# Optimization experiments

Measured on AMD Instinct MI355X. Metric: run time of the kernel, lower is better.

Reference implementation:

```python
import jax, jax.numpy as jnp
import numpy as np

N_WRD = 2000
WCODE = 3
EMB = 32
VSIZE = 7
VIEW = (16, 16)
B = 64
CSIZE = 128


def _vcode():
    # torch.meshgrid with default 'ij' indexing, cat -> (2, H*W) -> (H*W, 2)
    x = jnp.linspace(-1.0, 1.0, VIEW[0])
    y = jnp.linspace(-1.0, 1.0, VIEW[1])
    xg, yg = jnp.meshgrid(x, y, indexing='ij')
    return jnp.stack([xg.reshape(-1), yg.reshape(-1)], axis=-1)  # (V, 2)


def setup_inputs() -> dict:
    key = jax.random.key(0)
    ks = jax.random.split(key, 20)
    s = 0.02
    d = {
        'view_cell': jax.random.normal(ks[0], (B, CSIZE, VIEW[0] * VIEW[1]), jnp.float32),
        'v': jax.random.normal(ks[1], (B, VSIZE), jnp.float32),
        'w2c_w1': jax.random.normal(ks[2], (VSIZE, 512), jnp.float32) * s,
        'w2c_b1': jnp.zeros((512,), jnp.float32),
        'w2c_w2': jax.random.normal(ks[3], (512, WCODE * N_WRD), jnp.float32) * s,
        'w2c_b2': jnp.zeros((WCODE * N_WRD,), jnp.float32),
        'fc1_w': jax.random.normal(ks[4], (WCODE, 256), jnp.float32) * s,
        'fc1_b': jnp.zeros((256,), jnp.float32),
        'fc2_w': jax.random.normal(ks[5], (256, 256), jnp.float32) * s,
        'fc2_b': jnp.zeros((256,), jnp.float32),
        'fca_w': jax.random.normal(ks[6], (256, 1), jnp.float32) * s,
        'fca_b': jnp.zeros((1,), jnp.float32),
        'fce_w': jax.random.normal(ks[7], (256, EMB), jnp.float32) * s,
        'fce_b': jnp.zeros((EMB,), jnp.float32),
        'vse_w1': jax.random.normal(ks[8], (2, 128), jnp.float32) * s,
        'vse_b1': jnp.zeros((128,), jnp.float32),
        'vse_w2': jax.random.normal(ks[9], (128, EMB), jnp.float32) * s,
        'vse_b2': jnp.zeros((EMB,), jnp.float32),
    }
    return d


def reference(view_cell, v, w2c_w1, w2c_b1, w2c_w2, w2c_b2,
              fc1_w, fc1_b, fc2_w, fc2_b, fca_w, fca_b, fce_w, fce_b,
              vse_w1, vse_b1, vse_w2, vse_b2):
    b = v.shape[0]
    # w2c: v -> per-cell world codes
    h0 = jax.nn.relu(v @ w2c_w1 + w2c_b1)                     # (B, 512)
    wcode = (h0 @ w2c_w2 + w2c_b2).reshape(-1, WCODE)          # (B*N, 3)
    h = jax.nn.relu(wcode @ fc1_w + fc1_b)                     # (B*N, 256)
    h = jax.nn.relu(h @ fc2_w + fc2_b)
    activation = jax.nn.sigmoid(h @ fca_w + fca_b).reshape(b, N_WRD, 1)
    cs_emb = (h @ fce_w + fce_b).reshape(b, N_WRD, EMB)        # (B, N, E)
    # view-space embedding of the pixel grid
    vcode = _vcode()                                           # (V, 2)
    vs = jax.nn.relu(vcode @ vse_w1 + vse_b1) @ vse_w2 + vse_b2  # (V, E)
    # relation / gated softmax routing
    relation = jnp.einsum('bne,ve->bnv', cs_emb, vs)           # (B, N, V)
    route = jax.nn.softmax(relation, axis=2) * activation      # (B, N, V)
    # write: view_cell (B, C, V) @ route^T (B, V, N) -> (B, C, N)
    wrd_cell = jnp.einsum('bcv,bnv->bcn', view_cell, route)
    return wrd_cell
```

## Files before the change

### kernel.cpp

```cpp
#include <hip/hip_runtime.h>
#include <hip/hip_bf16.h>
#include <math.h>

#define NWRD 2000
#define BB 64
#define CS 128
#define VV 256

typedef __attribute__((ext_vector_type(8)))  short short8;
typedef __attribute__((ext_vector_type(16))) float f32x16;

#define WS_FC2WT 0
#define WS_WCODE (WS_FC2WT + 32768)
#define WS_VSB   (WS_WCODE + 384000)
#define WS_W2T   (WS_VSB + 4096)
#define WS_VCB   (WS_W2T + 1536000)
#define WS_FCEWT (WS_VCB + 1048576)
#define WS_H0B   (WS_FCEWT + 4096)
#define WS_FCAWB (WS_H0B + 16384)

__device__ __forceinline__ unsigned short f2bf(float x) {
    unsigned int u = __float_as_uint(x);
    u += 0x7fffu + ((u >> 16) & 1u);
    return (unsigned short)(u >> 16);
}

#define PREP_A 1024
#define PREP_B (PREP_A + 752)
#define PREP_C (PREP_B + 128)
#define PREP_D (PREP_C + 32)
#define PREP_E (PREP_D + 16)
#define PREP_N (PREP_E + 1)
__global__ __launch_bounds__(256) void kprep(
        const float* __restrict__ vc, unsigned short* __restrict__ vcb,
        const float* __restrict__ w2, unsigned short* __restrict__ w2T,
        const float* __restrict__ v, const float* __restrict__ w2c_w1,
        const float* __restrict__ w2c_b1, unsigned short* __restrict__ h0b,
        const float* __restrict__ vse_w1, const float* __restrict__ vse_b1,
        const float* __restrict__ vse_w2, const float* __restrict__ vse_b2,
        unsigned short* __restrict__ vsb,
        const float* __restrict__ fc2_w, unsigned short* __restrict__ fc2wT,
        const float* __restrict__ fce_w, unsigned short* __restrict__ fcewT,
        const float* __restrict__ fca_w, unsigned short* __restrict__ fcawB) {
    __shared__ unsigned short smem[9216];
    int bid = blockIdx.x, t = threadIdx.x;
    if (bid < PREP_A) {
        int i = (bid * 256 + t) * 8;
        float4 f0 = *(const float4*)(vc + i);
        float4 f1 = *(const float4*)(vc + i + 4);
        union { short8 v8; unsigned short u[8]; } o;
        o.u[0] = f2bf(f0.x); o.u[1] = f2bf(f0.y); o.u[2] = f2bf(f0.z); o.u[3] = f2bf(f0.w);
        o.u[4] = f2bf(f1.x); o.u[5] = f2bf(f1.y); o.u[6] = f2bf(f1.z); o.u[7] = f2bf(f1.w);
        *(short8*)(vcb + i) = o.v8;
    } else if (bid < PREP_B) {
        unsigned short (*tile)[66] = (unsigned short(*)[66])smem;
        int b2 = bid - PREP_A;
        int n0 = (b2 % 94) * 64, k0 = (b2 / 94) * 64;
        int nl = t & 63, kb = (t >> 6) * 16;
        int nc = (n0 + nl) < 6000 ? (n0 + nl) : 5999;
#pragma unroll
        for (int i = 0; i < 16; i++)
            tile[nl][kb + i] = f2bf(w2[(size_t)(k0 + kb + i)*6000 + nc]);
        __syncthreads();
        int kl = t & 63, nb = (t >> 6) * 16;
#pragma unroll
        for (int i = 0; i < 16; i++) {
            int nn = n0 + nb + i;
            if (nn < 6000) w2T[(size_t)nn*512 + k0 + kl] = tile[nb + i][kl];
        }
    } else if (bid < PREP_C) {
        int c = bid - PREP_B;
        int b = c >> 1, j = (c & 1)*256 + t;
        float s = w2c_b1[j];
#pragma unroll
        for (int k = 0; k < 7; k++) s = fmaf(v[b*7 + k], w2c_w1[k*512 + j], s);
        h0b[b*512 + j] = f2bf(fmaxf(s, 0.f));
    } else if (bid < PREP_D) {
        float* hs = (float*)smem;
        int blk = bid - PREP_C;
        int m = t & 127, half = t >> 7;
#pragma unroll
        for (int q = 0; q < 4; q++) {
            int vloc = half*4 + q;
            int vv = blk*8 + vloc;
            float x = (2.f/15.f)*(float)(vv >> 4) - 1.f;
            float y = (2.f/15.f)*(float)(vv & 15) - 1.f;
            float h = vse_b1[m] + x*vse_w1[m] + y*vse_w1[128 + m];
            hs[vloc*128 + m] = fmaxf(h, 0.f);
        }
        __syncthreads();
        int vloc = t >> 5, e = t & 31;
        float s = vse_b2[e];
        for (int mm = 0; mm < 128; mm++) s = fmaf(hs[vloc*128 + mm], vse_w2[mm*32 + e], s);
        vsb[(blk*8 + vloc)*32 + e] = f2bf(s);
    } else if (bid < PREP_E) {
        unsigned short (*tile)[72] = (unsigned short(*)[72])smem;
        int b2 = bid - PREP_D;
        int k0t = (b2 >> 2) * 64, n0t = (b2 & 3) * 64;
        int nl = t & 63, kb = (t >> 6) * 16;
#pragma unroll
        for (int i = 0; i < 16; i++)
            tile[kb + i][nl] = f2bf(fc2_w[(size_t)(k0t + kb + i)*256 + n0t + nl]);
        __syncthreads();
        int kl = t & 63, nb = (t >> 6) * 16;
#pragma unroll
        for (int i = 0; i < 16; i++)
            fc2wT[(size_t)(n0t + nb + i)*256 + k0t + kl] = tile[kl][nb + i];
    } else {
        int e = t & 31, kb = (t >> 5) * 32;
        unsigned short tmp[32];
#pragma unroll
        for (int i = 0; i < 32; i++) tmp[i] = f2bf(fce_w[(size_t)(kb + i)*32 + e]);
#pragma unroll
        for (int i = 0; i < 4; i++)
            *(short8*)(fcewT + (size_t)e*256 + kb + i*8) = *(short8*)(tmp + i*8);
#pragma unroll
        for (int i = 0; i < 32; i++)
            fcawB[(size_t)e*256 + kb + i] = (e == 0) ? f2bf(fca_w[kb + i]) : (unsigned short)0;
    }
}

__global__ __launch_bounds__(512) void k2_gemm(const unsigned short* __restrict__ h0b,
        const unsigned short* __restrict__ w2T, const float* __restrict__ b2,
        float* __restrict__ wcode) {
    int t = threadIdx.x;
    int w = t >> 6, lane = t & 63, l31 = lane & 31, h = lane >> 5;
    int mt = w & 1, nt = w >> 1;
    int n = blockIdx.x*128 + nt*32 + l31;
    int nc = n < 6000 ? n : 5999;
    f32x16 a0v, a1v;
#pragma unroll
    for (int i = 0; i < 16; i++) { a0v[i] = 0.f; a1v[i] = 0.f; }
#pragma unroll 8
    for (int ks = 0; ks < 16; ks++) {
        int k0 = ks*16 + h*8;
        short8 af0 = *(const short8*)(h0b + (mt*32 + l31)*512 + k0);
        short8 bf0 = *(const short8*)(w2T + (size_t)nc*512 + k0);
        a0v = __builtin_amdgcn_mfma_f32_32x32x16_bf16(af0, bf0, a0v, 0, 0, 0);
        short8 af1 = *(const short8*)(h0b + (mt*32 + l31)*512 + k0 + 256);
        short8 bf1 = *(const short8*)(w2T + (size_t)nc*512 + k0 + 256);
        a1v = __builtin_amdgcn_mfma_f32_32x32x16_bf16(af1, bf1, a1v, 0, 0, 0);
    }
    if (n < 6000) {
        float bias = b2[n];
#pragma unroll
        for (int i = 0; i < 16; i++) {
            int row = (i & 3) + 8*(i >> 2) + 4*h;
            wcode[(size_t)(mt*32 + row)*6000 + n] = a0v[i] + a1v[i] + bias;
        }
    }
}

#define K45_LDS 77056
__global__ __launch_bounds__(512, 4) void k45(
        const unsigned short* __restrict__ vcb,
        const float* __restrict__ wcode,
        const float* __restrict__ fc1_w, const float* __restrict__ fc1_b,
        const unsigned short* __restrict__ fc2wT, const float* __restrict__ fc2_b,
        const float* __restrict__ fca_b_p,
        const unsigned short* __restrict__ fcawB,
        const unsigned short* __restrict__ fcewT, const float* __restrict__ fce_b,
        const unsigned short* __restrict__ vsb,
        float* __restrict__ out) {
    extern __shared__ char lds[];
    unsigned short* h1b    = (unsigned short*)lds;
    unsigned short* h2b    = (unsigned short*)(lds + 33792);
    unsigned short* routeB = h2b;
    unsigned short* embL   = (unsigned short*)(lds + 67584);
    float* actL   = (float*)(lds + 72704);
    float* wcsAll = (float*)(lds + 72960);
    float* redS   = (float*)(lds + 76032);
    int t = threadIdx.x;
    int w = t >> 6, lane = t & 63, l31 = lane & 31, h = lane >> 5;
    int b = blockIdx.y;
    int n0 = blockIdx.x * 256;

    {
        const float* wb = wcode + (size_t)b*6000;
        int i0 = n0*3 + t;
        wcsAll[t] = wb[i0 < 6000 ? i0 : 5999];
        if (t < 256) {
            int i1 = n0*3 + 512 + t;
            wcsAll[512 + t] = wb[i1 < 6000 ? i1 : 5999];
        }
    }
    int jq = (t & 63) * 4;
    float4 wa  = *(const float4*)(fc1_w + jq);
    float4 wb4 = *(const float4*)(fc1_w + 256 + jq);
    float4 wc  = *(const float4*)(fc1_w + 512 + jq);
    float4 bb4 = *(const float4*)(fc1_b + jq);
    int mtA = w & 1, na = (w >> 1) * 32, nb2 = na + 128;
    float ba = fc2_b[na + l31], bbv = fc2_b[nb2 + l31];
    float be = fce_b[l31];
    float fcab = fca_b_p[0];
    int ntR = w & 1, vq = w >> 1;
    int ctE = w >> 1, ntE = w & 1;
    size_t arowE = ((size_t)(b*128 + ctE*32 + l31))*256;
    __syncthreads();

    for (int c = 0; c < 4; c++) {
        int w0 = n0 + c*64;
#pragma unroll
        for (int rr = 0; rr < 8; rr++) {
            int r = w*8 + rr;
            const float* wr = wcsAll + (c*64 + r)*3;
            float c0 = wr[0], c1 = wr[1], c2 = wr[2];
            float v0 = fmaxf(fmaf(c2, wc.x, fmaf(c1, wb4.x, fmaf(c0, wa.x, bb4.x))), 0.f);
            float v1 = fmaxf(fmaf(c2, wc.y, fmaf(c1, wb4.y, fmaf(c0, wa.y, bb4.y))), 0.f);
            float v2 = fmaxf(fmaf(c2, wc.z, fmaf(c1, wb4.z, fmaf(c0, wa.z, bb4.z))), 0.f);
            float v3 = fmaxf(fmaf(c2, wc.w, fmaf(c1, wb4.w, fmaf(c0, wa.w, bb4.w))), 0.f);
            uint2 p;
            p.x = (unsigned int)f2bf(v0) | ((unsigned int)f2bf(v1) << 16);
            p.y = (unsigned int)f2bf(v2) | ((unsigned int)f2bf(v3) << 16);
            *(uint2*)(h1b + r*264 + jq) = p;
        }
        __syncthreads();
        {
            f32x16 c0, c1;
#pragma unroll
            for (int i = 0; i < 16; i++) { c0[i] = 0.f; c1[i] = 0.f; }
#pragma unroll 4
            for (int ks = 0; ks < 16; ks++) {
                int k0 = ks*16 + h*8;
                short8 af  = *(const short8*)(h1b + (mtA*32 + l31)*264 + k0);
                short8 bfa = *(const short8*)(fc2wT + (size_t)(na  + l31)*256 + k0);
                short8 bfb = *(const short8*)(fc2wT + (size_t)(nb2 + l31)*256 + k0);
                c0 = __builtin_amdgcn_mfma_f32_32x32x16_bf16(af, bfa, c0, 0, 0, 0);
                c1 = __builtin_amdgcn_mfma_f32_32x32x16_bf16(af, bfb, c1, 0, 0, 0);
            }
#pragma unroll
            for (int i = 0; i < 16; i++) {
                int row = (i & 3) + 8*(i >> 2) + 4*h;
                h2b[(mtA*32 + row)*264 + na  + l31] = f2bf(fmaxf(c0[i] + ba, 0.f));
                h2b[(mtA*32 + row)*264 + nb2 + l31] = f2bf(fmaxf(c1[i] + bbv, 0.f));
            }
        }
        __syncthreads();
        if (w < 2) {
            f32x16 ce;
#pragma unroll
            for (int i = 0; i < 16; i++) ce[i] = 0.f;
#pragma unroll 4
            for (int ks = 0; ks < 16; ks++) {
                int k0 = ks*16 + h*8;
                short8 af = *(const short8*)(h2b + (w*32 + l31)*264 + k0);
                short8 bf = *(const short8*)(fcewT + (size_t)l31*256 + k0);
                ce = __builtin_amdgcn_mfma_f32_32x32x16_bf16(af, bf, ce, 0, 0, 0);
            }
#pragma unroll
            for (int i = 0; i < 16; i++) {
                int row = (i & 3) + 8*(i >> 2) + 4*h;
                embL[(w*32 + row)*40 + l31] = f2bf(ce[i] + be);
            }
        } else if (w < 4) {
            int m = w - 2;
            f32x16 ca;
#pragma unroll
            for (int i = 0; i < 16; i++) ca[i] = 0.f;
#pragma unroll 4
            for (int ks = 0; ks < 16; ks++) {
                int k0 = ks*16 + h*8;
                short8 af = *(const short8*)(h2b + (m*32 + l31)*264 + k0);
                short8 bf = *(const short8*)(fcawB + (size_t)l31*256 + k0);
                ca = __builtin_amdgcn_mfma_f32_32x32x16_bf16(af, bf, ca, 0, 0, 0);
            }
            if (l31 == 0) {
#pragma unroll
                for (int i = 0; i < 16; i++) {
                    int row = (i & 3) + 8*(i >> 2) + 4*h;
                    actL[m*32 + row] = 1.f / (1.f + __expf(-(ca[i] + fcab)));
                }
            }
        }
        __syncthreads();
        int nloc = ntR*32 + l31;
        f32x16 ra[2];
#pragma unroll
        for (int mt = 0; mt < 2; mt++)
#pragma unroll
            for (int i = 0; i < 16; i++) ra[mt][i] = 0.f;
#pragma unroll
        for (int s = 0; s < 2; s++) {
            short8 bfrag = *(const short8*)(embL + nloc*40 + s*16 + h*8);
#pragma unroll
            for (int mt = 0; mt < 2; mt++) {
                int vrow = (vq*2 + mt)*32 + l31;
                short8 afrag = *(const short8*)(vsb + vrow*32 + s*16 + h*8);
                ra[mt] = __builtin_amdgcn_mfma_f32_32x32x16_bf16(afrag, bfrag, ra[mt], 0, 0, 0);
            }
        }
        float sm = 0.f;
#pragma unroll
        for (int mt = 0; mt < 2; mt++)
#pragma unroll
            for (int i = 0; i < 16; i++) {
                float e = __expf(ra[mt][i]);
                ra[mt][i] = e;
                sm += e;
            }
        sm += __shfl_xor(sm, 32);
        if (lane < 32) redS[w*32 + l31] = sm;
        __syncthreads();
        sm = 0.f;
#pragma unroll
        for (int q = 0; q < 4; q++) sm += redS[(q*2 + ntR)*32 + l31];
        float scale = actL[nloc] / sm;
#pragma unroll
        for (int mt = 0; mt < 2; mt++) {
#pragma unroll
            for (int rp = 0; rp < 4; rp++) {
                int vb = (vq*2 + mt)*32 + rp*8 + h*4;
                unsigned int p0 = (unsigned int)f2bf(ra[mt][rp*4+0]*scale)
                                | ((unsigned int)f2bf(ra[mt][rp*4+1]*scale) << 16);
                unsigned int p1 = (unsigned int)f2bf(ra[mt][rp*4+2]*scale)
                                | ((unsigned int)f2bf(ra[mt][rp*4+3]*scale) << 16);
                *(uint2*)(routeB + nloc*264 + vb) = make_uint2(p0, p1);
            }
        }
        __syncthreads();
        {
            f32x16 cc;
#pragma unroll
            for (int i = 0; i < 16; i++) cc[i] = 0.f;
            const unsigned short* rrow = routeB + (ntE*32 + l31)*264;
#pragma unroll 4
            for (int ks = 0; ks < 16; ks++) {
                int k0 = ks*16 + h*8;
                short8 bf = *(const short8*)(rrow + k0);
                short8 a0 = *(const short8*)(vcb + arowE + k0);
                cc = __builtin_amdgcn_mfma_f32_32x32x16_bf16(a0, bf, cc, 0, 0, 0);
            }
            int ng = w0 + ntE*32 + l31;
            if (ng < NWRD) {
                float* ob = out + (size_t)b*128*NWRD + ng;
#pragma unroll
                for (int i = 0; i < 16; i++) {
                    int crow = (i & 3) + 8*(i >> 2) + 4*h;
                    ob[(size_t)(ctE*32 + crow)*NWRD] = cc[i];
                }
            }
        }
    }
}

extern "C" void kernel_launch(void* const* d_in, const int* in_sizes, int n_in,
                              void* d_out, int out_size, void* d_ws, size_t ws_size,
                              hipStream_t stream) {
    const float* view_cell = (const float*)d_in[0];
    const float* v       = (const float*)d_in[1];
    const float* w2c_w1  = (const float*)d_in[2];
    const float* w2c_b1  = (const float*)d_in[3];
    const float* w2c_w2  = (const float*)d_in[4];
    const float* w2c_b2  = (const float*)d_in[5];
    const float* fc1_w   = (const float*)d_in[6];
    const float* fc1_b   = (const float*)d_in[7];
    const float* fc2_w   = (const float*)d_in[8];
    const float* fc2_b   = (const float*)d_in[9];
    const float* fca_w   = (const float*)d_in[10];
    const float* fca_b   = (const float*)d_in[11];
    const float* fce_w   = (const float*)d_in[12];
    const float* fce_b   = (const float*)d_in[13];
    const float* vse_w1  = (const float*)d_in[14];
    const float* vse_b1  = (const float*)d_in[15];
    const float* vse_w2  = (const float*)d_in[16];
    const float* vse_b2  = (const float*)d_in[17];
    float* ws    = (float*)d_ws;
    unsigned short* fc2wT = (unsigned short*)(ws + WS_FC2WT);
    float* wcode = ws + WS_WCODE;
    unsigned short* vsb   = (unsigned short*)(ws + WS_VSB);
    unsigned short* w2T   = (unsigned short*)(ws + WS_W2T);
    unsigned short* vcb   = (unsigned short*)(ws + WS_VCB);
    unsigned short* fcewT = (unsigned short*)(ws + WS_FCEWT);
    unsigned short* h0b   = (unsigned short*)(ws + WS_H0B);
    unsigned short* fcawB = (unsigned short*)(ws + WS_FCAWB);
    float* out   = (float*)d_out;

    kprep<<<PREP_N, 256, 0, stream>>>(view_cell, vcb, w2c_w2, w2T,
                                      v, w2c_w1, w2c_b1, h0b,
                                      vse_w1, vse_b1, vse_w2, vse_b2, vsb,
                                      fc2_w, fc2wT, fce_w, fcewT, fca_w, fcawB);
    k2_gemm<<<47, 512, 0, stream>>>(h0b, w2T, w2c_b2, wcode);
    (void)hipFuncSetAttribute((const void*)k45,
                              hipFuncAttributeMaxDynamicSharedMemorySize, K45_LDS);
    dim3 g45(8, 64);
    k45<<<g45, 512, K45_LDS, stream>>>(vcb, wcode, fc1_w, fc1_b, fc2wT, fc2_b,
                                       fca_b, fcawB, fcewT, fce_b, vsb, out);
}
```

Before: 243.9 us.

## Fuse w2 transpose and h0 compute into LDS-staged GEMM; defer softmax normalization

Removes the separate w2 transpose and h0 passes through global workspace. A new kernel converts w2 columns to bf16 directly in LDS, computes h0 per block in LDS, and runs the full K=512 MFMA GEMM from LDS. Separately, the softmax normalization and activation scale are moved from the per-element route packing to the output epilogue, which removes one __syncthreads in k45. The trade-off is that h0 is recomputed in each of 94 blocks and the w2 reads are strided per column.

```diff
diff --git a/kernel.cpp b/kernel.cpp
--- a/kernel.cpp
+++ b/kernel.cpp
@@ -13,11 +13,9 @@
 #define WS_FC2WT 0
 #define WS_WCODE (WS_FC2WT + 32768)
 #define WS_VSB   (WS_WCODE + 384000)
-#define WS_W2T   (WS_VSB + 4096)
-#define WS_VCB   (WS_W2T + 1536000)
+#define WS_VCB   (WS_VSB + 4096)
 #define WS_FCEWT (WS_VCB + 1048576)
-#define WS_H0B   (WS_FCEWT + 4096)
-#define WS_FCAWB (WS_H0B + 16384)
+#define WS_FCAWB (WS_FCEWT + 4096)
 
 __device__ __forceinline__ unsigned short f2bf(float x) {
     unsigned int u = __float_as_uint(x);
@@ -25,17 +23,12 @@
     return (unsigned short)(u >> 16);
 }
 
-#define PREP_A 1024
-#define PREP_B (PREP_A + 752)
-#define PREP_C (PREP_B + 128)
-#define PREP_D (PREP_C + 32)
-#define PREP_E (PREP_D + 16)
-#define PREP_N (PREP_E + 1)
-__global__ __launch_bounds__(256) void kprep(
+#define PL_A 1024
+#define PL_B (PL_A + 32)
+#define PL_C (PL_B + 16)
+#define PL_N (PL_C + 1)
+__global__ __launch_bounds__(256) void kprep_light(
         const float* __restrict__ vc, unsigned short* __restrict__ vcb,
-        const float* __restrict__ w2, unsigned short* __restrict__ w2T,
-        const float* __restrict__ v, const float* __restrict__ w2c_w1,
-        const float* __restrict__ w2c_b1, unsigned short* __restrict__ h0b,
         const float* __restrict__ vse_w1, const float* __restrict__ vse_b1,
         const float* __restrict__ vse_w2, const float* __restrict__ vse_b2,
         unsigned short* __restrict__ vsb,
@@ -44,7 +37,7 @@
         const float* __restrict__ fca_w, unsigned short* __restrict__ fcawB) {
     __shared__ unsigned short smem[9216];
     int bid = blockIdx.x, t = threadIdx.x;
-    if (bid < PREP_A) {
+    if (bid < PL_A) {
         int i = (bid * 256 + t) * 8;
         float4 f0 = *(const float4*)(vc + i);
         float4 f1 = *(const float4*)(vc + i + 4);
@@ -52,32 +45,9 @@
         o.u[0] = f2bf(f0.x); o.u[1] = f2bf(f0.y); o.u[2] = f2bf(f0.z); o.u[3] = f2bf(f0.w);
         o.u[4] = f2bf(f1.x); o.u[5] = f2bf(f1.y); o.u[6] = f2bf(f1.z); o.u[7] = f2bf(f1.w);
         *(short8*)(vcb + i) = o.v8;
-    } else if (bid < PREP_B) {
-        unsigned short (*tile)[66] = (unsigned short(*)[66])smem;
-        int b2 = bid - PREP_A;
-        int n0 = (b2 % 94) * 64, k0 = (b2 / 94) * 64;
-        int nl = t & 63, kb = (t >> 6) * 16;
-        int nc = (n0 + nl) < 6000 ? (n0 + nl) : 5999;
-#pragma unroll
-        for (int i = 0; i < 16; i++)
-            tile[nl][kb + i] = f2bf(w2[(size_t)(k0 + kb + i)*6000 + nc]);
-        __syncthreads();
-        int kl = t & 63, nb = (t >> 6) * 16;
-#pragma unroll
-        for (int i = 0; i < 16; i++) {
-            int nn = n0 + nb + i;
-            if (nn < 6000) w2T[(size_t)nn*512 + k0 + kl] = tile[nb + i][kl];
-        }
-    } else if (bid < PREP_C) {
-        int c = bid - PREP_B;
-        int b = c >> 1, j = (c & 1)*256 + t;
-        float s = w2c_b1[j];
-#pragma unroll
-        for (int k = 0; k < 7; k++) s = fmaf(v[b*7 + k], w2c_w1[k*512 + j], s);
-        h0b[b*512 + j] = f2bf(fmaxf(s, 0.f));
-    } else if (bid < PREP_D) {
+    } else if (bid < PL_B) {
         float* hs = (float*)smem;
-        int blk = bid - PREP_C;
+        int blk = bid - PL_A;
         int m = t & 127, half = t >> 7;
 #pragma unroll
         for (int q = 0; q < 4; q++) {
@@ -93,9 +63,9 @@
         float s = vse_b2[e];
         for (int mm = 0; mm < 128; mm++) s = fmaf(hs[vloc*128 + mm], vse_w2[mm*32 + e], s);
         vsb[(blk*8 + vloc)*32 + e] = f2bf(s);
-    } else if (bid < PREP_E) {
+    } else if (bid < PL_C) {
         unsigned short (*tile)[72] = (unsigned short(*)[72])smem;
-        int b2 = bid - PREP_D;
+        int b2 = bid - PL_B;
         int k0t = (b2 >> 2) * 64, n0t = (b2 & 3) * 64;
         int nl = t & 63, kb = (t >> 6) * 16;
 #pragma unroll
@@ -120,33 +90,65 @@
     }
 }
 
-__global__ __launch_bounds__(512) void k2_gemm(const unsigned short* __restrict__ h0b,
-        const unsigned short* __restrict__ w2T, const float* __restrict__ b2,
-        float* __restrict__ wcode) {
+#define W2_LDS (64*520*2*2)
+__global__ __launch_bounds__(256) void kprep_w2(
+        const float* __restrict__ w2, const float* __restrict__ v,
+        const float* __restrict__ w2c_w1, const float* __restrict__ w2c_b1,
+        const float* __restrict__ w2c_b2, float* __restrict__ wcode) {
+    extern __shared__ char plds[];
+    unsigned short* h0L = (unsigned short*)plds;
+    unsigned short* w2L = (unsigned short*)(plds + 64*520*2);
     int t = threadIdx.x;
+    int n0 = blockIdx.x * 64;
+    {
+        int nl = t & 63, kq = t >> 6;
+        int ncl = (n0 + nl) < 6000 ? (n0 + nl) : 5999;
+#pragma unroll 4
+        for (int k = kq*128; k < kq*128 + 128; k += 2) {
+            unsigned int p = (unsigned int)f2bf(w2[(size_t)k*6000 + ncl])
+                           | ((unsigned int)f2bf(w2[(size_t)(k+1)*6000 + ncl]) << 16);
+            *(unsigned int*)(w2L + nl*520 + k) = p;
+        }
+    }
+    {
+        int j0 = t * 2;
+        float wk0[7], wk1[7];
+#pragma unroll
+        for (int k = 0; k < 7; k++) { wk0[k] = w2c_w1[k*512 + j0]; wk1[k] = w2c_w1[k*512 + j0 + 1]; }
+        float bb0 = w2c_b1[j0], bb1 = w2c_b1[j0 + 1];
+        for (int b = 0; b < 64; b++) {
+            float s0 = bb0, s1 = bb1;
+#pragma unroll
+            for (int k = 0; k < 7; k++) {
+                float vv = v[b*7 + k];
+                s0 = fmaf(vv, wk0[k], s0);
+                s1 = fmaf(vv, wk1[k], s1);
+            }
+            unsigned int p = (unsigned int)f2bf(fmaxf(s0, 0.f))
+                           | ((unsigned int)f2bf(fmaxf(s1, 0.f)) << 16);
+            *(unsigned int*)(h0L + b*520 + j0) = p;
+        }
+    }
+    __syncthreads();
     int w = t >> 6, lane = t & 63, l31 = lane & 31, h = lane >> 5;
     int mt = w & 1, nt = w >> 1;
-    int n = blockIdx.x*128 + nt*32 + l31;
-    int nc = n < 6000 ? n : 5999;
-    f32x16 a0v, a1v;
-#pragma unroll
-    for (int i = 0; i < 16; i++) { a0v[i] = 0.f; a1v[i] = 0.f; }
+    f32x16 acc;
+#pragma unroll
+    for (int i = 0; i < 16; i++) acc[i] = 0.f;
 #pragma unroll 8
-    for (int ks = 0; ks < 16; ks++) {
+    for (int ks = 0; ks < 32; ks++) {
         int k0 = ks*16 + h*8;
-        short8 af0 = *(const short8*)(h0b + (mt*32 + l31)*512 + k0);
-        short8 bf0 = *(const short8*)(w2T + (size_t)nc*512 + k0);
-        a0v = __builtin_amdgcn_mfma_f32_32x32x16_bf16(af0, bf0, a0v, 0, 0, 0);
-        short8 af1 = *(const short8*)(h0b + (mt*32 + l31)*512 + k0 + 256);
-        short8 bf1 = *(const short8*)(w2T + (size_t)nc*512 + k0 + 256);
-        a1v = __builtin_amdgcn_mfma_f32_32x32x16_bf16(af1, bf1, a1v, 0, 0, 0);
-    }
+        short8 af = *(const short8*)(h0L + (mt*32 + l31)*520 + k0);
+        short8 bf = *(const short8*)(w2L + (nt*32 + l31)*520 + k0);
+        acc = __builtin_amdgcn_mfma_f32_32x32x16_bf16(af, bf, acc, 0, 0, 0);
+    }
+    int n = n0 + nt*32 + l31;
     if (n < 6000) {
-        float bias = b2[n];
+        float bias = w2c_b2[n];
 #pragma unroll
         for (int i = 0; i < 16; i++) {
             int row = (i & 3) + 8*(i >> 2) + 4*h;
-            wcode[(size_t)(mt*32 + row)*6000 + n] = a0v[i] + a1v[i] + bias;
+            wcode[(size_t)(mt*32 + row)*6000 + n] = acc[i] + bias;
         }
     }
 }
@@ -300,20 +302,15 @@
             }
         sm += __shfl_xor(sm, 32);
         if (lane < 32) redS[w*32 + l31] = sm;
-        __syncthreads();
-        sm = 0.f;
-#pragma unroll
-        for (int q = 0; q < 4; q++) sm += redS[(q*2 + ntR)*32 + l31];
-        float scale = actL[nloc] / sm;
 #pragma unroll
         for (int mt = 0; mt < 2; mt++) {
 #pragma unroll
             for (int rp = 0; rp < 4; rp++) {
                 int vb = (vq*2 + mt)*32 + rp*8 + h*4;
-                unsigned int p0 = (unsigned int)f2bf(ra[mt][rp*4+0]*scale)
-                                | ((unsigned int)f2bf(ra[mt][rp*4+1]*scale) << 16);
-                unsigned int p1 = (unsigned int)f2bf(ra[mt][rp*4+2]*scale)
-                                | ((unsigned int)f2bf(ra[mt][rp*4+3]*scale) << 16);
+                unsigned int p0 = (unsigned int)f2bf(ra[mt][rp*4+0])
+                                | ((unsigned int)f2bf(ra[mt][rp*4+1]) << 16);
+                unsigned int p1 = (unsigned int)f2bf(ra[mt][rp*4+2])
+                                | ((unsigned int)f2bf(ra[mt][rp*4+3]) << 16);
                 *(uint2*)(routeB + nloc*264 + vb) = make_uint2(p0, p1);
             }
         }
@@ -330,13 +327,16 @@
                 short8 a0 = *(const short8*)(vcb + arowE + k0);
                 cc = __builtin_amdgcn_mfma_f32_32x32x16_bf16(a0, bf, cc, 0, 0, 0);
             }
+            float ssum = redS[ntE*32 + l31] + redS[(2 + ntE)*32 + l31]
+                       + redS[(4 + ntE)*32 + l31] + redS[(6 + ntE)*32 + l31];
+            float scl = actL[ntE*32 + l31] / ssum;
             int ng = w0 + ntE*32 + l31;
             if (ng < NWRD) {
                 float* ob = out + (size_t)b*128*NWRD + ng;
 #pragma unroll
                 for (int i = 0; i < 16; i++) {
                     int crow = (i & 3) + 8*(i >> 2) + 4*h;
-                    ob[(size_t)(ctE*32 + crow)*NWRD] = cc[i];
+                    ob[(size_t)(ctE*32 + crow)*NWRD] = cc[i] * scl;
                 }
             }
         }
@@ -368,18 +368,17 @@
     unsigned short* fc2wT = (unsigned short*)(ws + WS_FC2WT);
     float* wcode = ws + WS_WCODE;
     unsigned short* vsb   = (unsigned short*)(ws + WS_VSB);
-    unsigned short* w2T   = (unsigned short*)(ws + WS_W2T);
     unsigned short* vcb   = (unsigned short*)(ws + WS_VCB);
     unsigned short* fcewT = (unsigned short*)(ws + WS_FCEWT);
-    unsigned short* h0b   = (unsigned short*)(ws + WS_H0B);
     unsigned short* fcawB = (unsigned short*)(ws + WS_FCAWB);
     float* out   = (float*)d_out;
 
-    kprep<<<PREP_N, 256, 0, stream>>>(view_cell, vcb, w2c_w2, w2T,
-                                      v, w2c_w1, w2c_b1, h0b,
-                                      vse_w1, vse_b1, vse_w2, vse_b2, vsb,
-                                      fc2_w, fc2wT, fce_w, fcewT, fca_w, fcawB);
-    k2_gemm<<<47, 512, 0, stream>>>(h0b, w2T, w2c_b2, wcode);
+    kprep_light<<<PL_N, 256, 0, stream>>>(view_cell, vcb,
+                                          vse_w1, vse_b1, vse_w2, vse_b2, vsb,
+                                          fc2_w, fc2wT, fce_w, fcewT, fca_w, fcawB);
+    (void)hipFuncSetAttribute((const void*)kprep_w2,
+                              hipFuncAttributeMaxDynamicSharedMemorySize, W2_LDS);
+    kprep_w2<<<94, 256, W2_LDS, stream>>>(w2c_w2, v, w2c_w1, w2c_b1, w2c_b2, wcode);
     (void)hipFuncSetAttribute((const void*)k45,
                               hipFuncAttributeMaxDynamicSharedMemorySize, K45_LDS);
     dim3 g45(8, 64);
```

Result: no change. 244.6 us (+0.3%).
